# Kernel tuning notes

Measured on AMD Instinct MI355X. Metric: run time of the kernel, lower is better.

The kernel has to match this reference:

```python
import jax, jax.numpy as jnp
import numpy as np

DIM = 1024
HEADS = 16
DIM_HEAD = 64
SCALE = DIM_HEAD ** -0.5


def setup_inputs() -> dict:
    key = jax.random.key(0)
    ks = jax.random.split(key, 7)
    init = lambda k, shape: jax.random.normal(k, shape, dtype=jnp.float32) * (shape[0] ** -0.5)
    return {
        "x": jax.random.normal(ks[0], (4, 4096, DIM), dtype=jnp.float32),
        "Wq": init(ks[1], (DIM, HEADS * DIM_HEAD)),
        "Wk": init(ks[2], (DIM, HEADS * DIM_HEAD)),
        "Wv": init(ks[3], (DIM, HEADS * DIM_HEAD)),
        "Wg": init(ks[4], (DIM, HEADS * DIM_HEAD)),
        "bg": jnp.zeros((HEADS * DIM_HEAD,), dtype=jnp.float32),
        "Wo": init(ks[5], (HEADS * DIM_HEAD, DIM)),
    }


def _split_heads(t):
    b, n, _ = t.shape
    return t.reshape(b, n, HEADS, DIM_HEAD).transpose(0, 2, 1, 3)  # b h n d


def reference(x, Wq, Wk, Wv, Wg, bg, Wo):
    # projections
    q = _split_heads(x @ Wq)
    k = _split_heads(x @ Wk)
    v = _split_heads(x @ Wv)
    g = _split_heads(x @ Wg + bg)

    # feature map + gate
    q = jax.nn.elu(q) + 1.0
    k = jax.nn.elu(k) + 1.0
    g = jax.nn.sigmoid(g)

    # linear attention: per-head kv state, no n x n scores
    kv = jnp.einsum("bhnd,bhne->bhde", k, v)          # [b,h,d,d]
    k_sum = k.sum(axis=-2)                              # [b,h,d]
    z = 1.0 / jnp.clip(jnp.einsum("bhnd,bhd->bhn", q, k_sum), 1e-6)
    out = jnp.einsum("bhnd,bhde->bhne", q * SCALE, kv)
    out = out * z[..., None] * g                        # [b,h,n,d]

    b, h, n, d = out.shape
    out = out.transpose(0, 2, 1, 3).reshape(b, n, h * d)
    return out @ Wo
```

## Files before the change

### kernel.cpp

```cpp
#include <hip/hip_runtime.h>
#include <math.h>

#define DIM 1024
#define SCALE 0.125f
#define NT 16

typedef __attribute__((ext_vector_type(8))) short bh8;
typedef __attribute__((ext_vector_type(4))) short bh4;
typedef __attribute__((ext_vector_type(4))) float f4v;

__device__ __forceinline__ unsigned short f2bf(float f) {
  unsigned u = __builtin_bit_cast(unsigned, f);
  return (unsigned short)((u + 0x7FFFu + ((u >> 16) & 1u)) >> 16);
}
__device__ __forceinline__ float bf2f(unsigned short u) {
  return __builtin_bit_cast(float, (unsigned)u << 16);
}
__device__ __forceinline__ float elu1(float v) {
  return v > 0.f ? v + 1.f : __expf(v);
}
__device__ __forceinline__ f4v mfma16(bh8 a, bh8 b, f4v c) {
  return __builtin_amdgcn_mfma_f32_16x16x32_bf16(a, b, c, 0, 0, 0);
}

typedef const void __attribute__((address_space(1)))* gas1_t;
typedef void __attribute__((address_space(3)))* las3_t;

__device__ __forceinline__ bh8 frag(const unsigned short* lds, int row, int k8) {
  const int q = ((row << 3) | k8) ^ (row & 7);
  return *reinterpret_cast<const bh8*>(lds + q * 8);
}

__device__ __forceinline__ void gll_tile(const unsigned short* g, int ldg,
                                         unsigned short* lds, int t) {
  const int lane = t & 63, w = t >> 6;
#pragma unroll
  for (int cc = 0; cc < 4; ++cc) {
    const int base = (w * 4 + cc) * 64;
    const int q = base + lane;
    const int c = q ^ ((q >> 3) & 7);
    __builtin_amdgcn_global_load_lds(
        (gas1_t)(const void*)(g + (size_t)(c >> 3) * ldg + (c & 7) * 8),
        (las3_t)(void*)(lds + (size_t)base * 8), 16, 0, 0);
  }
}

__global__ __launch_bounds__(256) void p0(const float* __restrict__ x,
                                          unsigned short* __restrict__ xb) {
  const size_t i = ((size_t)blockIdx.x * 256 + threadIdx.x) * 8;
  const float4 a = *reinterpret_cast<const float4*>(x + i);
  const float4 b = *reinterpret_cast<const float4*>(x + i + 4);
  bh8 v;
  v[0] = (short)f2bf(a.x); v[1] = (short)f2bf(a.y);
  v[2] = (short)f2bf(a.z); v[3] = (short)f2bf(a.w);
  v[4] = (short)f2bf(b.x); v[5] = (short)f2bf(b.y);
  v[6] = (short)f2bf(b.z); v[7] = (short)f2bf(b.w);
  *reinterpret_cast<bh8*>(xb + i) = v;
}

__global__ __launch_bounds__(256) void p1(
    const float* __restrict__ Wq, const float* __restrict__ Wk,
    const float* __restrict__ Wv, const float* __restrict__ Wg,
    const float* __restrict__ Wo, unsigned short* __restrict__ WallT,
    unsigned short* __restrict__ WoT) {
  const int m = blockIdx.z;
  const int tc = blockIdx.x, tr = blockIdx.y;
  const int t = threadIdx.x;
  const float* src = m == 0 ? Wq : m == 1 ? Wk : m == 2 ? Wv : m == 3 ? Wg : Wo;
  __shared__ float tile[64][65];
#pragma unroll
  for (int i = 0; i < 4; ++i) {
    const int idx = i * 256 + t;
    const int r = idx >> 4;
    const int c4 = (idx & 15) * 4;
    const float4 v = *reinterpret_cast<const float4*>(
        src + (size_t)(tr * 64 + r) * DIM + tc * 64 + c4);
    tile[r][c4] = v.x; tile[r][c4 + 1] = v.y;
    tile[r][c4 + 2] = v.z; tile[r][c4 + 3] = v.w;
  }
  __syncthreads();
  unsigned short* dst = (m < 4) ? WallT : WoT;
#pragma unroll
  for (int i = 0; i < 4; ++i) {
    const int idx = i * 256 + t;
    const int lc = idx >> 4;
    const int k4i = (idx & 15) * 4;
    const size_t drow = (m < 4) ? (size_t)(tc * 256 + m * 64 + lc)
                                : (size_t)(tc * 64 + lc);
    bh4 v;
#pragma unroll
    for (int jj = 0; jj < 4; ++jj) v[jj] = (short)f2bf(tile[k4i + jj][lc]);
    *reinterpret_cast<bh4*>(dst + drow * DIM + tr * 64 + k4i) = v;
  }
}

template <int MODE>
__global__ __launch_bounds__(512, 2) void gemm8(
    const unsigned short* __restrict__ gA,
    const unsigned short* __restrict__ gB, const float* __restrict__ bg,
    unsigned short* __restrict__ ob, float* __restrict__ of) {
  const int t = threadIdx.x, lane = t & 63, w = t >> 6;
  const int wr = w >> 2, wc = w & 3, g4 = lane >> 4, c0 = lane & 15;
  const int nwg = gridDim.x;
  const int NBC = (MODE == 0) ? 16 : 4;
  const int rbn = nwg / NBC;
  const int bid = (int)blockIdx.x;
  const int xcd = bid & 7;
  const int idx = bid >> 3;
  const int bandsz = rbn >> 3;
  const int cb = idx / bandsz;
  const int rb = xcd * bandsz + (idx - cb * bandsz);

  constexpr int LDGA = (MODE == 0) ? 1024 : 4096;
  constexpr int ASTR = (MODE == 0) ? 64 : 256;
  constexpr int AOFF = (MODE == 0) ? 0 : 64;

  __shared__ __align__(16) unsigned short lds[65536];

  int offA[2], offB[2], dstc[2];
#pragma unroll
  for (int cc = 0; cc < 2; ++cc) {
    const int base = (w * 2 + cc) * 64;
    const int q = base + lane;
    const int c = q ^ ((q >> 3) & 7);
    offA[cc] = (c >> 3) * LDGA + (c & 7) * 8;
    offB[cc] = (c >> 3) * 1024 + (c & 7) * 8;
    dstc[cc] = base * 8;
  }
  const unsigned short* Abase = gA + (size_t)rb * 256 * LDGA + AOFF;
  const unsigned short* Bbase = gB + (size_t)cb * 256 * 1024;

#define SA(kt, half)                                                          \
  {                                                                           \
    _Pragma("unroll") for (int cc = 0; cc < 2; ++cc)                          \
        __builtin_amdgcn_global_load_lds(                                     \
            (gas1_t)(Abase + (size_t)(half) * 128 * LDGA + offA[cc] +         \
                     (kt) * ASTR),                                            \
            (las3_t)(lds + ((kt) & 1) * 16384 + (half) * 8192 + dstc[cc]),    \
            16, 0, 0);                                                        \
  }
#define SB(kt, half)                                                          \
  {                                                                           \
    _Pragma("unroll") for (int cc = 0; cc < 2; ++cc)                          \
        __builtin_amdgcn_global_load_lds(                                     \
            (gas1_t)(Bbase + (size_t)(half) * 128 * 1024 + offB[cc] +         \
                     (kt) * 64),                                              \
            (las3_t)(lds + 32768 + ((kt) & 1) * 16384 + (half) * 8192 +       \
                     dstc[cc]),                                               \
            16, 0, 0);                                                        \
  }

  f4v acc[8][4];
#pragma unroll
  for (int i = 0; i < 8; ++i)
#pragma unroll
    for (int j = 0; j < 4; ++j) acc[i][j] = (f4v){0.f, 0.f, 0.f, 0.f};

  SB(0, 0); SB(0, 1); SA(0, 0); SA(0, 1); SB(1, 0); SB(1, 1);

#pragma unroll 2
  for (int kt = 0; kt < NT; ++kt) {
    if (kt < NT - 1) {
      asm volatile("s_waitcnt vmcnt(4)" ::: "memory");
    } else {
      asm volatile("s_waitcnt vmcnt(0)" ::: "memory");
    }
    __builtin_amdgcn_sched_barrier(0);
    __builtin_amdgcn_s_barrier();
    const unsigned short* Ah = lds + (kt & 1) * 16384 + wr * 8192;
    const unsigned short* Bh =
        lds + 32768 + (kt & 1) * 16384 + (wc >> 1) * 8192;
    const int br0 = (wc & 1) * 64;

    bh8 bfr[4][2], a0[2][2];
#pragma unroll
    for (int nf = 0; nf < 4; ++nf)
#pragma unroll
      for (int kf = 0; kf < 2; ++kf)
        bfr[nf][kf] = frag(Bh, br0 + nf * 16 + c0, kf * 4 + g4);
#pragma unroll
    for (int i = 0; i < 2; ++i)
#pragma unroll
      for (int kf = 0; kf < 2; ++kf)
        a0[i][kf] = frag(Ah, i * 16 + c0, kf * 4 + g4);
    if (kt + 1 < NT) { SA(kt + 1, 0); SA(kt + 1, 1); }
    __builtin_amdgcn_s_barrier();
    __builtin_amdgcn_s_setprio(1);
#pragma unroll
    for (int i = 0; i < 2; ++i)
#pragma unroll
      for (int nf = 0; nf < 4; ++nf)
#pragma unroll
        for (int kf = 0; kf < 2; ++kf)
          acc[i][nf] = mfma16(bfr[nf][kf], a0[i][kf], acc[i][nf]);
    __builtin_amdgcn_s_setprio(0);
    __builtin_amdgcn_s_barrier();

    bh8 a1[2][2];
#pragma unroll
    for (int i = 0; i < 2; ++i)
#pragma unroll
      for (int kf = 0; kf < 2; ++kf)
        a1[i][kf] = frag(Ah, (2 + i) * 16 + c0, kf * 4 + g4);
    if (kt + 2 < NT) SB(kt + 2, 0);
    __builtin_amdgcn_s_barrier();
    __builtin_amdgcn_s_setprio(1);
#pragma unroll
    for (int i = 0; i < 2; ++i)
#pragma unroll
      for (int nf = 0; nf < 4; ++nf)
#pragma unroll
        for (int kf = 0; kf < 2; ++kf)
          acc[2 + i][nf] = mfma16(bfr[nf][kf], a1[i][kf], acc[2 + i][nf]);
    __builtin_amdgcn_s_setprio(0);
    __builtin_amdgcn_s_barrier();

    bh8 a2[2][2];
#pragma unroll
    for (int i = 0; i < 2; ++i)
#pragma unroll
      for (int kf = 0; kf < 2; ++kf)
        a2[i][kf] = frag(Ah, (4 + i) * 16 + c0, kf * 4 + g4);
    if (kt + 2 < NT) SB(kt + 2, 1);
    __builtin_amdgcn_s_barrier();
    __builtin_amdgcn_s_setprio(1);
#pragma unroll
    for (int i = 0; i < 2; ++i)
#pragma unroll
      for (int nf = 0; nf < 4; ++nf)
#pragma unroll
        for (int kf = 0; kf < 2; ++kf)
          acc[4 + i][nf] = mfma16(bfr[nf][kf], a2[i][kf], acc[4 + i][nf]);
    __builtin_amdgcn_s_setprio(0);
    __builtin_amdgcn_s_barrier();

    bh8 a3[2][2];
#pragma unroll
    for (int i = 0; i < 2; ++i)
#pragma unroll
      for (int kf = 0; kf < 2; ++kf)
        a3[i][kf] = frag(Ah, (6 + i) * 16 + c0, kf * 4 + g4);
    __builtin_amdgcn_s_barrier();
    __builtin_amdgcn_s_setprio(1);
#pragma unroll
    for (int i = 0; i < 2; ++i)
#pragma unroll
      for (int nf = 0; nf < 4; ++nf)
#pragma unroll
        for (int kf = 0; kf < 2; ++kf)
          acc[6 + i][nf] = mfma16(bfr[nf][kf], a3[i][kf], acc[6 + i][nf]);
    __builtin_amdgcn_s_setprio(0);
  }
#undef SA
#undef SB

  if (MODE == 0) {
    float bgv[4][4];
    if (wc == 3) {
#pragma unroll
      for (int nf = 0; nf < 4; ++nf) {
        const float4 bv =
            *reinterpret_cast<const float4*>(bg + cb * 64 + nf * 16 + g4 * 4);
        bgv[nf][0] = bv.x; bgv[nf][1] = bv.y;
        bgv[nf][2] = bv.z; bgv[nf][3] = bv.w;
      }
    }
#pragma unroll
    for (int rf = 0; rf < 8; ++rf) {
      const size_t row = (size_t)rb * 256 + wr * 128 + rf * 16 + c0;
#pragma unroll
      for (int nf = 0; nf < 4; ++nf) {
        ushort4 o;
#pragma unroll
        for (int r = 0; r < 4; ++r) {
          float v = acc[rf][nf][r];
          if (wc <= 1) v = elu1(v);
          else if (wc == 3) v = 1.f / (1.f + __expf(-(v + bgv[nf][r])));
          ((unsigned short*)&o)[r] = f2bf(v);
        }
        *reinterpret_cast<ushort4*>(
            ob + row * 4096 + cb * 256 + wc * 64 + nf * 16 + g4 * 4) = o;
      }
    }
  } else {
#pragma unroll
    for (int rf = 0; rf < 8; ++rf) {
      const size_t row = (size_t)rb * 256 + wr * 128 + rf * 16 + c0;
#pragma unroll
      for (int nf = 0; nf < 4; ++nf) {
        float4 o;
        o.x = acc[rf][nf][0]; o.y = acc[rf][nf][1];
        o.z = acc[rf][nf][2]; o.w = acc[rf][nf][3];
        *reinterpret_cast<float4*>(
            of + row * DIM + cb * 256 + wc * 64 + nf * 16 + g4 * 4) = o;
      }
    }
  }
}

__global__ __launch_bounds__(256) void g2(const unsigned short* __restrict__ qkvg,
                                          float* __restrict__ kv_part,
                                          float* __restrict__ ksum_part) {
  const int h = blockIdx.x, z = blockIdx.y;
  const int bb = z >> 5, sp = z & 31;
  const int t = threadIdx.x, ti = t >> 4, tj = t & 15;
  __shared__ unsigned short s[128 * 128];
  float kvacc[4][4] = {{0.f}};
  float ksacc[4] = {0.f, 0.f, 0.f, 0.f};
  const unsigned short* src =
      qkvg + ((size_t)bb * 4096 + sp * 128) * 4096 + h * 256 + 64;
#pragma unroll
  for (int it = 0; it < 8; ++it) {
    const int idx = it * 256 + t;
    const int r = idx >> 4, c8 = idx & 15;
    *reinterpret_cast<bh8*>(&s[r * 128 + c8 * 8]) =
        *reinterpret_cast<const bh8*>(src + (size_t)r * 4096 + c8 * 8);
  }
  __syncthreads();
  for (int r = 0; r < 128; ++r) {
    const bh4 k4 = *reinterpret_cast<const bh4*>(&s[r * 128 + 4 * ti]);
    const bh4 v4 = *reinterpret_cast<const bh4*>(&s[r * 128 + 64 + 4 * tj]);
    float kf[4], vf[4];
#pragma unroll
    for (int i = 0; i < 4; ++i) {
      kf[i] = bf2f((unsigned short)k4[i]);
      vf[i] = bf2f((unsigned short)v4[i]);
      ksacc[i] += kf[i];
    }
#pragma unroll
    for (int i = 0; i < 4; ++i)
#pragma unroll
      for (int j = 0; j < 4; ++j) kvacc[i][j] = fmaf(kf[i], vf[j], kvacc[i][j]);
  }
  float* kp = kv_part + (((size_t)(bb * 16 + h)) * 32 + sp) * 4096;
#pragma unroll
  for (int i = 0; i < 4; ++i)
#pragma unroll
    for (int j = 0; j < 4; ++j) kp[(4 * ti + i) * 64 + 4 * tj + j] = kvacc[i][j];
  if (tj == 0) {
#pragma unroll
    for (int i = 0; i < 4; ++i)
      ksum_part[(((size_t)(bb * 16 + h)) * 32 + sp) * 64 + 4 * ti + i] = ksacc[i];
  }
}

__global__ __launch_bounds__(256) void g2r(const float* __restrict__ kv_part,
                                           const float* __restrict__ ksum_part,
                                           unsigned short* __restrict__ kvT,
                                           float* __restrict__ ksum, int b0) {
  const int bhl = blockIdx.x, t = threadIdx.x;
  const size_t bh = (size_t)b0 * 16 + bhl;
#pragma unroll
  for (int i = 0; i < 16; ++i) {
    const int idx = i * 256 + t;
    const int d = idx >> 6, e = idx & 63;
    float s = 0.f;
    for (int sp = 0; sp < 32; ++sp)
      s += kv_part[((size_t)bhl * 32 + sp) * 4096 + idx];
    kvT[bh * 4096 + e * 64 + d] = f2bf(s);
  }
  if (t < 64) {
    float s = 0.f;
    for (int sp = 0; sp < 32; ++sp)
      s += ksum_part[((size_t)bhl * 32 + sp) * 64 + t];
    ksum[bh * 64 + t] = s;
  }
}

__global__ __launch_bounds__(256) void g3(unsigned short* __restrict__ qkvg,
                                          const unsigned short* __restrict__ kvT,
                                          const float* __restrict__ ksum,
                                          int b0) {
  const int h = blockIdx.x, z = blockIdx.y;
  const int t = threadIdx.x, lane = t & 63, w = t >> 6;
  const int g4 = lane >> 4, c0 = lane & 15;
  __shared__ unsigned short sQ[8192];
  __shared__ unsigned short skv[64 * 72];
  __shared__ float sks[64], sden[128];
  const int bb = z >> 5;
  const size_t bh = (size_t)(b0 + bb) * 16 + h;
  for (int i = t; i < 4096; i += 256)
    skv[(i >> 6) * 72 + (i & 63)] = kvT[bh * 4096 + i];
  if (t < 64) sks[t] = ksum[bh * 64 + t];
  const size_t row0 = (size_t)z * 128;
  gll_tile(qkvg + row0 * 4096 + h * 256, 4096, sQ, t);
  __syncthreads();
  if (t < 128) {
    float s = 0.f;
    for (int d = 0; d < 64; ++d)
      s += bf2f(sQ[((((t) << 3) | (d >> 3)) ^ (t & 7)) * 8 + (d & 7)]) * sks[d];
    sden[t] = SCALE / fmaxf(s, 1e-6f);
  }
  __syncthreads();
  f4v oacc[2][4];
#pragma unroll
  for (int ii = 0; ii < 2; ++ii)
#pragma unroll
    for (int et = 0; et < 4; ++et) oacc[ii][et] = (f4v){0.f, 0.f, 0.f, 0.f};
#pragma unroll
  for (int kf = 0; kf < 2; ++kf) {
    bh8 aq[2];
#pragma unroll
    for (int ii = 0; ii < 2; ++ii)
      aq[ii] = frag(sQ, w * 32 + ii * 16 + c0, kf * 4 + g4);
#pragma unroll
    for (int et = 0; et < 4; ++et) {
      const bh8 bkv = *reinterpret_cast<const bh8*>(
          skv + (et * 16 + c0) * 72 + kf * 32 + g4 * 8);
#pragma unroll
      for (int ii = 0; ii < 2; ++ii)
        oacc[ii][et] = mfma16(aq[ii], bkv, oacc[ii][et]);
    }
  }
#pragma unroll
  for (int ii = 0; ii < 2; ++ii)
#pragma unroll
    for (int et = 0; et < 4; ++et)
#pragma unroll
      for (int r = 0; r < 4; ++r) {
        const int row = w * 32 + ii * 16 + g4 * 4 + r;
        const int e = et * 16 + c0;
        const float gv = bf2f(qkvg[(row0 + row) * 4096 + h * 256 + 192 + e]);
        qkvg[(row0 + row) * 4096 + h * 256 + 64 + e] =
            f2bf(oacc[ii][et][r] * sden[row] * gv);
      }
}

extern "C" void kernel_launch(void* const* d_in, const int* in_sizes, int n_in,
                              void* d_out, int out_size, void* d_ws,
                              size_t ws_size, hipStream_t stream) {
  const float* x  = (const float*)d_in[0];
  const float* Wq = (const float*)d_in[1];
  const float* Wk = (const float*)d_in[2];
  const float* Wv = (const float*)d_in[3];
  const float* Wg = (const float*)d_in[4];
  const float* bg = (const float*)d_in[5];
  const float* Wo = (const float*)d_in[6];
  float* out = (float*)d_out;
  char* w = (char*)d_ws;

  int nbat = 1;
  if (ws_size >= 11026432ull + 4ull * 50462720ull) nbat = 4;
  else if (ws_size >= 11026432ull + 2ull * 50462720ull) nbat = 2;

  unsigned short* WallT = (unsigned short*)(w);
  unsigned short* WoT   = (unsigned short*)(w + 8388608);
  unsigned short* kvT   = (unsigned short*)(w + 10485760);
  float*          ksum  = (float*)(w + 11010048);
  char* dyn = w + 11026432;
  float* kv_part        = (float*)dyn;
  float* ksum_part      = (float*)(dyn + (size_t)nbat * 8388608);
  unsigned short* xb    = (unsigned short*)(dyn + (size_t)nbat * (8388608 + 131072));
  unsigned short* qkvg  = (unsigned short*)(dyn + (size_t)nbat * (8388608 + 131072 + 8388608));

  p1<<<dim3(16, 16, 5), 256, 0, stream>>>(Wq, Wk, Wv, Wg, Wo, WallT, WoT);

  for (int b0 = 0; b0 < 4; b0 += nbat) {
    const int rows_p = nbat * 4096;
    p0<<<rows_p / 2, 256, 0, stream>>>(x + (size_t)b0 * 4096 * DIM, xb);
    gemm8<0><<<dim3((rows_p / 256) * 16), 512, 0, stream>>>(xb, WallT, bg,
                                                            qkvg, nullptr);
    g2<<<dim3(16, nbat * 32), 256, 0, stream>>>(qkvg, kv_part, ksum_part);
    g2r<<<nbat * 16, 256, 0, stream>>>(kv_part, ksum_part, kvT, ksum, b0);
    g3<<<dim3(16, nbat * 32), 256, 0, stream>>>(qkvg, kvT, ksum, b0);
    gemm8<1><<<dim3((rows_p / 256) * 4), 512, 0, stream>>>(
        qkvg, WoT, nullptr, nullptr, out + (size_t)b0 * 4096 * DIM);
  }
}
```

Baseline: 312.1 us.

## Fuse KV-state and k-sum reduction into projection GEMM epilogue via MFMA

```diff
diff --git a/kernel.cpp b/kernel.cpp
--- a/kernel.cpp
+++ b/kernel.cpp
@@ -98,7 +98,8 @@
 __global__ __launch_bounds__(512, 2) void gemm8(
     const unsigned short* __restrict__ gA,
     const unsigned short* __restrict__ gB, const float* __restrict__ bg,
-    unsigned short* __restrict__ ob, float* __restrict__ of) {
+    unsigned short* __restrict__ ob, float* __restrict__ of,
+    float* __restrict__ kv_part, float* __restrict__ ksum_part) {
   const int t = threadIdx.x, lane = t & 63, w = t >> 6;
   const int wr = w >> 2, wc = w & 3, g4 = lane >> 4, c0 = lane & 15;
   const int nwg = gridDim.x;
@@ -282,6 +283,57 @@
             ob + row * 4096 + cb * 256 + wc * 64 + nf * 16 + g4 * 4) = o;
       }
     }
+
+    __syncthreads();
+    if (wc == 1 || wc == 2) {
+      unsigned short* dstT = lds + (wc == 2 ? 16896 : 0);
+#pragma unroll
+      for (int rf = 0; rf < 8; ++rf) {
+        const int n = wr * 128 + rf * 16 + c0;
+#pragma unroll
+        for (int nf = 0; nf < 4; ++nf)
+#pragma unroll
+          for (int r = 0; r < 4; ++r) {
+            float v = acc[rf][nf][r];
+            if (wc == 1) v = elu1(v);
+            dstT[(nf * 16 + g4 * 4 + r) * 264 + n] = f2bf(v);
+          }
+      }
+    }
+    __syncthreads();
+    const unsigned short* kT = lds;
+    const unsigned short* vT = lds + 16896;
+    const size_t pbase = (size_t)((rb >> 4) * 16 + cb) * 16 + (rb & 15);
+#pragma unroll
+    for (int pi = 0; pi < 2; ++pi) {
+      const int p = w * 2 + pi, dt = p >> 2, et = p & 3;
+      f4v a = (f4v){0.f, 0.f, 0.f, 0.f};
+#pragma unroll
+      for (int kn = 0; kn < 8; ++kn) {
+        const bh8 kq = *reinterpret_cast<const bh8*>(
+            kT + (dt * 16 + c0) * 264 + kn * 32 + g4 * 8);
+        const bh8 vq = *reinterpret_cast<const bh8*>(
+            vT + (et * 16 + c0) * 264 + kn * 32 + g4 * 8);
+        a = mfma16(vq, kq, a);
+      }
+      float4 o;
+      o.x = a[0]; o.y = a[1]; o.z = a[2]; o.w = a[3];
+      *reinterpret_cast<float4*>(
+          kv_part + pbase * 4096 + (dt * 16 + c0) * 64 + et * 16 + g4 * 4) = o;
+    }
+    if (w < 4) {
+      bh8 ones;
+#pragma unroll
+      for (int j = 0; j < 8; ++j) ones[j] = (short)0x3F80;
+      f4v a = (f4v){0.f, 0.f, 0.f, 0.f};
+#pragma unroll
+      for (int kn = 0; kn < 8; ++kn) {
+        const bh8 kq = *reinterpret_cast<const bh8*>(
+            kT + (w * 16 + c0) * 264 + kn * 32 + g4 * 8);
+        a = mfma16(ones, kq, a);
+      }
+      if (lane < 16) ksum_part[pbase * 64 + w * 16 + c0] = a[0];
+    }
   } else {
 #pragma unroll
     for (int rf = 0; rf < 8; ++rf) {
@@ -298,52 +350,6 @@
   }
 }
 
-__global__ __launch_bounds__(256) void g2(const unsigned short* __restrict__ qkvg,
-                                          float* __restrict__ kv_part,
-                                          float* __restrict__ ksum_part) {
-  const int h = blockIdx.x, z = blockIdx.y;
-  const int bb = z >> 5, sp = z & 31;
-  const int t = threadIdx.x, ti = t >> 4, tj = t & 15;
-  __shared__ unsigned short s[128 * 128];
-  float kvacc[4][4] = {{0.f}};
-  float ksacc[4] = {0.f, 0.f, 0.f, 0.f};
-  const unsigned short* src =
-      qkvg + ((size_t)bb * 4096 + sp * 128) * 4096 + h * 256 + 64;
-#pragma unroll
-  for (int it = 0; it < 8; ++it) {
-    const int idx = it * 256 + t;
-    const int r = idx >> 4, c8 = idx & 15;
-    *reinterpret_cast<bh8*>(&s[r * 128 + c8 * 8]) =
-        *reinterpret_cast<const bh8*>(src + (size_t)r * 4096 + c8 * 8);
-  }
-  __syncthreads();
-  for (int r = 0; r < 128; ++r) {
-    const bh4 k4 = *reinterpret_cast<const bh4*>(&s[r * 128 + 4 * ti]);
-    const bh4 v4 = *reinterpret_cast<const bh4*>(&s[r * 128 + 64 + 4 * tj]);
-    float kf[4], vf[4];
-#pragma unroll
-    for (int i = 0; i < 4; ++i) {
-      kf[i] = bf2f((unsigned short)k4[i]);
-      vf[i] = bf2f((unsigned short)v4[i]);
-      ksacc[i] += kf[i];
-    }
-#pragma unroll
-    for (int i = 0; i < 4; ++i)
-#pragma unroll
-      for (int j = 0; j < 4; ++j) kvacc[i][j] = fmaf(kf[i], vf[j], kvacc[i][j]);
-  }
-  float* kp = kv_part + (((size_t)(bb * 16 + h)) * 32 + sp) * 4096;
-#pragma unroll
-  for (int i = 0; i < 4; ++i)
-#pragma unroll
-    for (int j = 0; j < 4; ++j) kp[(4 * ti + i) * 64 + 4 * tj + j] = kvacc[i][j];
-  if (tj == 0) {
-#pragma unroll
-    for (int i = 0; i < 4; ++i)
-      ksum_part[(((size_t)(bb * 16 + h)) * 32 + sp) * 64 + 4 * ti + i] = ksacc[i];
-  }
-}
-
 __global__ __launch_bounds__(256) void g2r(const float* __restrict__ kv_part,
                                            const float* __restrict__ ksum_part,
                                            unsigned short* __restrict__ kvT,
@@ -355,14 +361,14 @@
     const int idx = i * 256 + t;
     const int d = idx >> 6, e = idx & 63;
     float s = 0.f;
-    for (int sp = 0; sp < 32; ++sp)
-      s += kv_part[((size_t)bhl * 32 + sp) * 4096 + idx];
+    for (int sp = 0; sp < 16; ++sp)
+      s += kv_part[((size_t)bhl * 16 + sp) * 4096 + idx];
     kvT[bh * 4096 + e * 64 + d] = f2bf(s);
   }
   if (t < 64) {
     float s = 0.f;
-    for (int sp = 0; sp < 32; ++sp)
-      s += ksum_part[((size_t)bhl * 32 + sp) * 64 + t];
+    for (int sp = 0; sp < 16; ++sp)
+      s += ksum_part[((size_t)bhl * 16 + sp) * 64 + t];
     ksum[bh * 64 + t] = s;
   }
 }
@@ -385,11 +391,16 @@
   const size_t row0 = (size_t)z * 128;
   gll_tile(qkvg + row0 * 4096 + h * 256, 4096, sQ, t);
   __syncthreads();
-  if (t < 128) {
+  {
+    const int rr = t >> 1, hf = t & 1;
     float s = 0.f;
-    for (int d = 0; d < 64; ++d)
-      s += bf2f(sQ[((((t) << 3) | (d >> 3)) ^ (t & 7)) * 8 + (d & 7)]) * sks[d];
-    sden[t] = SCALE / fmaxf(s, 1e-6f);
+#pragma unroll
+    for (int dd = 0; dd < 32; ++dd) {
+      const int d = hf * 32 + dd;
+      s += bf2f(sQ[(((rr << 3) | (d >> 3)) ^ (rr & 7)) * 8 + (d & 7)]) * sks[d];
+    }
+    s += __shfl_xor(s, 1, 64);
+    if (hf == 0) sden[rr] = SCALE / fmaxf(s, 1e-6f);
   }
   __syncthreads();
   f4v oacc[2][4];
@@ -409,21 +420,26 @@
           skv + (et * 16 + c0) * 72 + kf * 32 + g4 * 8);
 #pragma unroll
       for (int ii = 0; ii < 2; ++ii)
-        oacc[ii][et] = mfma16(aq[ii], bkv, oacc[ii][et]);
-    }
-  }
-#pragma unroll
-  for (int ii = 0; ii < 2; ++ii)
-#pragma unroll
-    for (int et = 0; et < 4; ++et)
-#pragma unroll
-      for (int r = 0; r < 4; ++r) {
-        const int row = w * 32 + ii * 16 + g4 * 4 + r;
-        const int e = et * 16 + c0;
-        const float gv = bf2f(qkvg[(row0 + row) * 4096 + h * 256 + 192 + e]);
-        qkvg[(row0 + row) * 4096 + h * 256 + 64 + e] =
-            f2bf(oacc[ii][et][r] * sden[row] * gv);
-      }
+        oacc[ii][et] = mfma16(bkv, aq[ii], oacc[ii][et]);
+    }
+  }
+#pragma unroll
+  for (int ii = 0; ii < 2; ++ii) {
+    const int n = w * 32 + ii * 16 + c0;
+    const float z2 = sden[n];
+    const size_t rowbase = (row0 + n) * 4096 + h * 256;
+#pragma unroll
+    for (int et = 0; et < 4; ++et) {
+      const ushort4 gt = *reinterpret_cast<const ushort4*>(
+          qkvg + rowbase + 192 + et * 16 + g4 * 4);
+      ushort4 o;
+#pragma unroll
+      for (int r = 0; r < 4; ++r)
+        ((unsigned short*)&o)[r] =
+            f2bf(oacc[ii][et][r] * z2 * bf2f(((const unsigned short*)&gt)[r]));
+      *reinterpret_cast<ushort4*>(qkvg + rowbase + 64 + et * 16 + g4 * 4) = o;
+    }
+  }
 }
 
 extern "C" void kernel_launch(void* const* d_in, const int* in_sizes, int n_in,
@@ -439,9 +455,10 @@
   float* out = (float*)d_out;
   char* w = (char*)d_ws;
 
+  const size_t PB = 46202880ull;
   int nbat = 1;
-  if (ws_size >= 11026432ull + 4ull * 50462720ull) nbat = 4;
-  else if (ws_size >= 11026432ull + 2ull * 50462720ull) nbat = 2;
+  if (ws_size >= 11026432ull + 4ull * PB) nbat = 4;
+  else if (ws_size >= 11026432ull + 2ull * PB) nbat = 2;
 
   unsigned short* WallT = (unsigned short*)(w);
   unsigned short* WoT   = (unsigned short*)(w + 8388608);
@@ -449,21 +466,21 @@
   float*          ksum  = (float*)(w + 11010048);
   char* dyn = w + 11026432;
   float* kv_part        = (float*)dyn;
-  float* ksum_part      = (float*)(dyn + (size_t)nbat * 8388608);
-  unsigned short* xb    = (unsigned short*)(dyn + (size_t)nbat * (8388608 + 131072));
-  unsigned short* qkvg  = (unsigned short*)(dyn + (size_t)nbat * (8388608 + 131072 + 8388608));
+  float* ksum_part      = (float*)(dyn + (size_t)nbat * 4194304);
+  unsigned short* xb    = (unsigned short*)(dyn + (size_t)nbat * (4194304 + 65536));
+  unsigned short* qkvg  = (unsigned short*)(dyn + (size_t)nbat * (4194304 + 65536 + 8388608));
 
   p1<<<dim3(16, 16, 5), 256, 0, stream>>>(Wq, Wk, Wv, Wg, Wo, WallT, WoT);
 
   for (int b0 = 0; b0 < 4; b0 += nbat) {
     const int rows_p = nbat * 4096;
     p0<<<rows_p / 2, 256, 0, stream>>>(x + (size_t)b0 * 4096 * DIM, xb);
-    gemm8<0><<<dim3((rows_p / 256) * 16), 512, 0, stream>>>(xb, WallT, bg,
-                                                            qkvg, nullptr);
-    g2<<<dim3(16, nbat * 32), 256, 0, stream>>>(qkvg, kv_part, ksum_part);
+    gemm8<0><<<dim3((rows_p / 256) * 16), 512, 0, stream>>>(
+        xb, WallT, bg, qkvg, nullptr, kv_part, ksum_part);
     g2r<<<nbat * 16, 256, 0, stream>>>(kv_part, ksum_part, kvT, ksum, b0);
     g3<<<dim3(16, nbat * 32), 256, 0, stream>>>(qkvg, kvT, ksum, b0);
     gemm8<1><<<dim3((rows_p / 256) * 4), 512, 0, stream>>>(
-        qkvg, WoT, nullptr, nullptr, out + (size_t)b0 * 4096 * DIM);
-  }
-}
+        qkvg, WoT, nullptr, nullptr, out + (size_t)b0 * 4096 * DIM,
+        nullptr, nullptr);
+  }
+}
```

Result: faster. 296.7 us (-4.9%).
